# Optimization experiments

Measured on AMD Instinct MI355X. Metric: run time of the kernel, lower is better.

## Reference

```python
import jax, jax.numpy as jnp
import numpy as np

EPS = 1e-5  # torch LayerNorm default
NUM_HEADS = 8


def layernorm(x, g, b):
    m = jnp.mean(x, axis=-1, keepdims=True)
    v = jnp.var(x, axis=-1, keepdims=True)
    return (x - m) * jax.lax.rsqrt(v + EPS) * g + b


def dwconv(x_img, w, b):
    # x_img: [B,C,H,W]; w: [C,1,k,k] depthwise, 'same' padding
    C = x_img.shape[1]
    k = w.shape[-1]
    out = jax.lax.conv_general_dilated(
        x_img, w, (1, 1), [(k // 2, k // 2)] * 2,
        dimension_numbers=('NCHW', 'OIHW', 'NCHW'), feature_group_count=C)
    return out + b[None, :, None, None]


def _forward(x, domain_label, cpe_w, cpe_b, ln1_g, ln1_b, qkv_w, proj_w, proj_b,
             dl_w1, dl_b1, dl_w2, dl_b2, crpe_w3, crpe_b3, crpe_w5, crpe_b5,
             crpe_w7, crpe_b7, ln2_g, ln2_b, fc1_w, fc1_b, fc2_w, fc2_b, H, W, d):
    B, N, C = x.shape
    h = NUM_HEADS
    Ch = C // h
    scale = Ch ** (-0.5)

    # ---- CPE: depthwise 3x3 conv positional encoding with residual ----
    xi = x.transpose(0, 2, 1).reshape(B, C, H, W)
    xi = dwconv(xi, cpe_w, cpe_b) + xi
    x = xi.reshape(B, C, N).transpose(0, 2, 1)

    # ---- domain-indexed LayerNorm 1 (d is a static python int) ----
    cur = layernorm(x, ln1_g[d], ln1_b[d])

    # ---- factorized attention ----
    qkv = (cur @ qkv_w).reshape(B, N, 3, h, Ch).transpose(2, 0, 3, 1, 4)
    q, k, v = qkv[0], qkv[1], qkv[2]          # each [B,h,N,Ch]
    k_sm = jax.nn.softmax(k, axis=2)          # softmax over tokens
    kv = jnp.einsum('bhnk,bhnv->bhkv', k_sm, v)       # [B,h,Ch,Ch]
    factor_att = jnp.einsum('bhnk,bhkv->bhnv', q, kv)  # [B,h,N,Ch]

    # ---- conv relative position encoding (window splits {3:2,5:3,7:3}) ----
    v_img = v.transpose(0, 1, 3, 2).reshape(B, C, H, W)
    g1 = dwconv(v_img[:, :2 * Ch], crpe_w3, crpe_b3)
    g2 = dwconv(v_img[:, 2 * Ch:5 * Ch], crpe_w5, crpe_b5)
    g3 = dwconv(v_img[:, 5 * Ch:], crpe_w7, crpe_b7)
    conv_v = jnp.concatenate([g1, g2, g3], axis=1)        # [B,C,H,W]
    conv_v = conv_v.reshape(B, h, Ch, N).transpose(0, 1, 3, 2)
    crpe = q * conv_v                                      # [B,h,N,Ch]

    factor_att = scale * factor_att + crpe

    # ---- per-domain softmax gating over heads ----
    da = jax.nn.relu(domain_label @ dl_w1 + dl_b1) @ dl_w2 + dl_b2  # [B, h*Ch]
    da = da.reshape(B, h, Ch)[:, :, None, :]                        # [B,h,1,Ch]
    da = jax.nn.softmax(da, axis=1)                                  # over heads
    attn = (da * factor_att).transpose(0, 2, 1, 3).reshape(B, N, C)
    attn = attn @ proj_w + proj_b

    x = x + attn

    # ---- domain-indexed LayerNorm 2 + MLP ----
    cur = layernorm(x, ln2_g[d], ln2_b[d])
    cur = jax.nn.gelu(cur @ fc1_w + fc1_b, approximate=False) @ fc2_w + fc2_b
    return x + cur


def setup_inputs() -> dict:
    key = jax.random.key(0)
    ks = iter(jax.random.split(key, 32))
    B, H, W, C, h, nd = 8, 56, 56, 256, 8, 4
    N = H * W
    Ch = C // h
    hid = C // 2   # domain MLP hidden = max(dim//r,4), r=2
    mh = 4 * C     # mlp_ratio=4
    r = lambda shape, s=0.02: jax.random.normal(next(ks), shape, jnp.float32) * s
    return dict(
        x=jax.random.normal(next(ks), (B, N, C), jnp.float32),
        domain_label=jax.nn.one_hot(
            jax.random.randint(next(ks), (B,), 0, nd), nd, dtype=jnp.float32),
        cpe_w=r((C, 1, 3, 3)), cpe_b=jnp.zeros((C,), jnp.float32),
        ln1_g=jnp.ones((nd, C), jnp.float32), ln1_b=jnp.zeros((nd, C), jnp.float32),
        qkv_w=r((C, 3 * C)),
        proj_w=r((C, C)), proj_b=jnp.zeros((C,), jnp.float32),
        dl_w1=r((nd, hid)), dl_b1=jnp.zeros((hid,), jnp.float32),
        dl_w2=r((hid, C)), dl_b2=jnp.zeros((C,), jnp.float32),
        crpe_w3=r((2 * Ch, 1, 3, 3)), crpe_b3=jnp.zeros((2 * Ch,), jnp.float32),
        crpe_w5=r((3 * Ch, 1, 5, 5)), crpe_b5=jnp.zeros((3 * Ch,), jnp.float32),
        crpe_w7=r((3 * Ch, 1, 7, 7)), crpe_b7=jnp.zeros((3 * Ch,), jnp.float32),
        ln2_g=jnp.ones((nd, C), jnp.float32), ln2_b=jnp.zeros((nd, C), jnp.float32),
        fc1_w=r((C, mh)), fc1_b=jnp.zeros((mh,), jnp.float32),
        fc2_w=r((mh, C)), fc2_b=jnp.zeros((C,), jnp.float32),
        H=H, W=W, d=0,
    )


def reference(x, domain_label, cpe_w, cpe_b, ln1_g, ln1_b, qkv_w, proj_w, proj_b,
              dl_w1, dl_b1, dl_w2, dl_b2, crpe_w3, crpe_b3, crpe_w5, crpe_b5,
              crpe_w7, crpe_b7, ln2_g, ln2_b, fc1_w, fc1_b, fc2_w, fc2_b, H, W, d):
    return _forward(x, domain_label, cpe_w, cpe_b, ln1_g, ln1_b, qkv_w, proj_w,
                    proj_b, dl_w1, dl_b1, dl_w2, dl_b2, crpe_w3, crpe_b3, crpe_w5,
                    crpe_b5, crpe_w7, crpe_b7, ln2_g, ln2_b, fc1_w, fc1_b, fc2_w,
                    fc2_b, H, W, d)
```

## Files before the change

kernel.cpp:

```cpp
#include <hip/hip_runtime.h>
#include <hip/hip_bf16.h>
#include <math.h>

#define BB 8
#define HH 56
#define WW 56
#define NN (HH*WW)
#define CC 256
#define NH 8
#define NT (BB*NN)
#define HID 128
#define MH 1024
#define SCALE 0.17677669529663687f

typedef __attribute__((ext_vector_type(8))) short bf16x8;
typedef __attribute__((ext_vector_type(4))) float f32x4;

__device__ __forceinline__ ushort f2bf(float f) {
    __hip_bfloat16 h = __float2bfloat16(f);
    return *(ushort*)&h;
}
__device__ __forceinline__ uint pk2(float lo, float hi) {
    return ((uint)f2bf(hi) << 16) | (uint)f2bf(lo);
}
__device__ __forceinline__ float unlo(uint u) { return __uint_as_float(u << 16); }
__device__ __forceinline__ float unhi(uint u) { return __uint_as_float(u & 0xFFFF0000u); }

__device__ __forceinline__ void gload16(const void* g, void* s) {
    __builtin_amdgcn_global_load_lds(
        (const __attribute__((address_space(1))) void*)g,
        (__attribute__((address_space(3))) void*)s, 16, 0, 0);
}

__global__ __launch_bounds__(256) void wtrans_kernel(
    const float* __restrict__ w, ushort* __restrict__ wt, int K, int N)
{
    int idx = blockIdx.x * 256 + threadIdx.x;
    if (idx >= K * N) return;
    int n = idx / K, k = idx - n * K;
    wt[idx] = f2bf(w[(size_t)k * N + n]);
}

__global__ __launch_bounds__(256) void cpe_kernel(
    const float* __restrict__ x, const float* __restrict__ w,
    const float* __restrict__ bias, float* __restrict__ out)
{
    __shared__ uint vt[3 * 34 * 32];
    const int qq = blockIdx.x >> 1, hx = blockIdx.x & 1;
    const int y = blockIdx.y, b = blockIdx.z;
    const int c0 = qq * 64, x0 = hx * 28;
    const int t = threadIdx.x;
    const int p = t & 31;
    for (int rr = 0; rr < 3; ++rr) {
        int gy = y + rr - 1;
        const float* src = x + ((size_t)b * NN + gy * 56) * CC + c0;
        for (int lc = t >> 5; lc < 34; lc += 8) {
            int gx = x0 + lc - 3;
            float vlo = 0.f, vhi = 0.f;
            if ((unsigned)gy < 56u && (unsigned)gx < 56u) {
                vlo = src[(size_t)gx * CC + p];
                vhi = src[(size_t)gx * CC + p + 32];
            }
            vt[(rr * 34 + lc) * 32 + p] = pk2(vlo, vhi);
        }
    }
    uint wp[9];
    {
        const float* wl = w + (c0 + p) * 9;
        const float* wh = w + (c0 + 32 + p) * 9;
        #pragma unroll
        for (int i = 0; i < 9; ++i) wp[i] = pk2(wl[i], wh[i]);
    }
    const float blo = bias[c0 + p], bhi = bias[c0 + 32 + p];
    __syncthreads();

    const int wv = t >> 6, th = (t >> 5) & 1;
    int txl[4]; float clo[4], chi[4];
    #pragma unroll
    for (int jj = 0; jj < 4; ++jj) {
        int j = wv + jj * 4; if (j > 13) j = 13;
        txl[jj] = 2 * j + th;
        clo[jj] = blo; chi[jj] = bhi;
    }
    #pragma unroll
    for (int dy = 0; dy < 3; ++dy)
        #pragma unroll
        for (int dx = 0; dx < 3; ++dx) {
            const uint wpk = wp[dy * 3 + dx];
            const float wl = unlo(wpk), wh = unhi(wpk);
            #pragma unroll
            for (int jj = 0; jj < 4; ++jj) {
                uint vv = vt[(dy * 34 + txl[jj] + 2 + dx) * 32 + p];
                clo[jj] = fmaf(unlo(vv), wl, clo[jj]);
                chi[jj] = fmaf(unhi(vv), wh, chi[jj]);
            }
        }
    #pragma unroll
    for (int jj = 0; jj < 4; ++jj) {
        size_t tokg = (size_t)b * NN + y * 56 + x0 + txl[jj];
        const float* row = x + tokg * CC;
        out[tokg * CC + c0 + p]      = clo[jj] + row[c0 + p];
        out[tokg * CC + c0 + 32 + p] = chi[jj] + row[c0 + 32 + p];
    }
}

__global__ __launch_bounds__(256) void ln_kernel(
    const float* __restrict__ src, const float* __restrict__ g_all,
    const float* __restrict__ b_all, const int* __restrict__ dptr,
    ushort* __restrict__ dst)
{
    const int wid = threadIdx.x >> 6, lane = threadIdx.x & 63;
    const int row = blockIdx.x * 4 + wid;
    const int d = *dptr;
    const float* g = g_all + d * CC;
    const float* be = b_all + d * CC;
    const float* p = src + (size_t)row * CC;
    float4 v = *(const float4*)(p + lane * 4);
    float s = v.x + v.y + v.z + v.w;
    float sq = v.x*v.x + v.y*v.y + v.z*v.z + v.w*v.w;
    #pragma unroll
    for (int off = 1; off < 64; off <<= 1) {
        s  += __shfl_xor(s, off);
        sq += __shfl_xor(sq, off);
    }
    const float mean = s * (1.f / CC);
    const float var = sq * (1.f / CC) - mean * mean;
    const float rs = rsqrtf(var + 1e-5f);
    float4 g4 = *(const float4*)(g + lane * 4);
    float4 b4 = *(const float4*)(be + lane * 4);
    ushort4 o4;
    o4.x = f2bf((v.x - mean) * rs * g4.x + b4.x);
    o4.y = f2bf((v.y - mean) * rs * g4.y + b4.y);
    o4.z = f2bf((v.z - mean) * rs * g4.z + b4.z);
    o4.w = f2bf((v.w - mean) * rs * g4.w + b4.w);
    *(ushort4*)(dst + (size_t)row * CC + lane * 4) = o4;
}

template<int EPI>
__global__ __launch_bounds__(256) void gemm_mfma(
    const ushort* __restrict__ A, const ushort* __restrict__ Bt,
    const float* __restrict__ bias, const float* __restrict__ res,
    void* __restrict__ Cv, int M, int N, int K)
{
    __shared__ __align__(16) ushort Als[128 * 32];
    __shared__ __align__(16) ushort Bls[128 * 32];
    const int t = threadIdx.x;
    const int bm = blockIdx.y, bn = blockIdx.x;
    const int brow = bm * 128, bcol = bn * 128;
    const int lane = t & 63, w = t >> 6;
    const int wr = w >> 1, wc = w & 1;
    const int lrow = lane & 15, lko = (lane >> 4) * 8;

    const ushort* gA0 = A + (size_t)(brow + (t >> 2)) * K + (t & 3) * 8;
    const ushort* gA1 = gA0 + (size_t)64 * K;
    const ushort* gB0 = Bt + (size_t)(bcol + (t >> 2)) * K + (t & 3) * 8;
    const ushort* gB1 = gB0 + (size_t)64 * K;
    ushort* lA0 = &Als[t * 8];  ushort* lA1 = &Als[64 * 32 + t * 8];
    ushort* lB0 = &Bls[t * 8];  ushort* lB1 = &Bls[64 * 32 + t * 8];

    f32x4 acc[4][4] = {};

    for (int kt = 0; kt < K; kt += 32) {
        gload16(gA0 + kt, lA0);
        gload16(gA1 + kt, lA1);
        gload16(gB0 + kt, lB0);
        gload16(gB1 + kt, lB1);
        __syncthreads();
        bf16x8 af[4], bfr[4];
        #pragma unroll
        for (int i = 0; i < 4; ++i)
            af[i] = *(const bf16x8*)&Als[(wr * 64 + i * 16 + lrow) * 32 + lko];
        #pragma unroll
        for (int j = 0; j < 4; ++j)
            bfr[j] = *(const bf16x8*)&Bls[(wc * 64 + j * 16 + lrow) * 32 + lko];
        #pragma unroll
        for (int i = 0; i < 4; ++i)
            #pragma unroll
            for (int j = 0; j < 4; ++j)
                acc[i][j] = __builtin_amdgcn_mfma_f32_16x16x32_bf16(
                    af[i], bfr[j], acc[i][j], 0, 0, 0);
        __syncthreads();
    }

    float* Cf = (float*)Cv;
    ushort* Ch = (ushort*)Cv;
    #pragma unroll
    for (int j = 0; j < 4; ++j) {
        const int col = bcol + wc * 64 + j * 16 + lrow;
        const float bv = (EPI >= 2) ? bias[col] : 0.f;
        #pragma unroll
        for (int i = 0; i < 4; ++i) {
            const int row0 = brow + wr * 64 + i * 16 + (lane >> 4) * 4;
            #pragma unroll
            for (int r = 0; r < 4; ++r) {
                float v = acc[i][j][r] + bv;
                size_t off = (size_t)(row0 + r) * N + col;
                if (EPI == 2) {
                    v = 0.5f * v * (1.f + erff(v * 0.70710678118654752f));
                    Ch[off] = f2bf(v);
                } else if (EPI == 3) {
                    Cf[off] = v + res[off];
                } else {
                    Cf[off] = v;
                }
            }
        }
    }
}

__global__ __launch_bounds__(256) void kmax1_kernel(
    const float* __restrict__ qkv, float* __restrict__ pmax)
{
    const int chunk = blockIdx.x, b = blockIdx.y, c = threadIdx.x;
    const float* kb = qkv + (size_t)(b * NN + chunk * 98) * 768 + 256 + c;
    float m = -3.4e38f;
    for (int i = 0; i < 98; ++i) m = fmaxf(m, kb[(size_t)i * 768]);
    pmax[(b * 32 + chunk) * CC + c] = m;
}

__global__ __launch_bounds__(256) void kmax2_kernel(
    const float* __restrict__ pmax, float* __restrict__ cmax)
{
    const int b = blockIdx.x, c = threadIdx.x;
    float m = -3.4e38f;
    #pragma unroll
    for (int i = 0; i < 32; ++i) m = fmaxf(m, pmax[(b * 32 + i) * CC + c]);
    cmax[b * CC + c] = m;
}

__global__ __launch_bounds__(256) void kvacc_kernel(
    const float* __restrict__ qkv, const float* __restrict__ cmax,
    float* __restrict__ partial, float* __restrict__ psum)
{
    const int chunk = blockIdx.x, h = blockIdx.y, b = blockIdx.z;
    const int t = threadIdx.x;
    const int ck = t & 31, g = t >> 5;
    const int n0 = chunk * 196;
    const float* kb = qkv + (size_t)(b * NN + n0) * 768 + 256 + h * 32 + ck;
    const float* vb = qkv + (size_t)(b * NN + n0) * 768 + 512 + h * 32 + g * 4;
    const float cm = cmax[b * CC + h * 32 + ck];
    float a0 = 0.f, a1 = 0.f, a2 = 0.f, a3 = 0.f, s = 0.f;
    for (int i = 0; i < 196; ++i) {
        float e = __expf(kb[(size_t)i * 768] - cm);
        float4 v4 = *(const float4*)(vb + (size_t)i * 768);
        a0 += e * v4.x; a1 += e * v4.y; a2 += e * v4.z; a3 += e * v4.w;
        s += e;
    }
    float4 o = {a0, a1, a2, a3};
    *(float4*)(partial + ((((size_t)chunk * 8 + b) * 8 + h) * 32 + ck) * 32 + g * 4) = o;
    if (g == 0) psum[((chunk * 8 + b) * 8 + h) * 32 + ck] = s;
}

__global__ __launch_bounds__(256) void kvnorm_kernel(
    const float* __restrict__ partial, const float* __restrict__ psum,
    float* __restrict__ kv)
{
    const int idx = blockIdx.x * 256 + threadIdx.x;
    const int ckidx = idx >> 5;
    float sum = 0.f, cs = 0.f;
    #pragma unroll
    for (int ch = 0; ch < 16; ++ch) {
        sum += partial[(size_t)ch * 65536 + idx];
        cs  += psum[ch * 2048 + ckidx];
    }
    kv[idx] = sum / cs;
}

__global__ __launch_bounds__(256) void fa_kernel(
    float* __restrict__ qkv, const float* __restrict__ kvb)
{
    const int mt = blockIdx.x, h = blockIdx.y, b = blockIdx.z;
    const int t = threadIdx.x;
    const int lane = t & 63, wv = t >> 6;
    const int row0 = mt * 448 + wv * 112;
    const int lr = lane & 15, lk = (lane >> 4) * 8;

    bf16x8 bfr[2];
    #pragma unroll
    for (int jj = 0; jj < 2; ++jj)
        #pragma unroll
        for (int e = 0; e < 8; ++e)
            bfr[jj][e] = (short)f2bf(kvb[((size_t)(b * 8 + h) * 32 + lk + e) * 32 + jj * 16 + lr]);

    #pragma unroll
    for (int i = 0; i < 7; ++i) {
        size_t tok = (size_t)b * NN + row0 + i * 16 + lr;
        const float* qp = qkv + tok * 768 + h * 32 + lk;
        float4 qa = *(const float4*)qp;
        float4 qb2 = *(const float4*)(qp + 4);
        bf16x8 af;
        af[0] = (short)f2bf(qa.x);  af[1] = (short)f2bf(qa.y);
        af[2] = (short)f2bf(qa.z);  af[3] = (short)f2bf(qa.w);
        af[4] = (short)f2bf(qb2.x); af[5] = (short)f2bf(qb2.y);
        af[6] = (short)f2bf(qb2.z); af[7] = (short)f2bf(qb2.w);
        f32x4 a0 = {0.f, 0.f, 0.f, 0.f}, a1 = {0.f, 0.f, 0.f, 0.f};
        a0 = __builtin_amdgcn_mfma_f32_16x16x32_bf16(af, bfr[0], a0, 0, 0, 0);
        a1 = __builtin_amdgcn_mfma_f32_16x16x32_bf16(af, bfr[1], a1, 0, 0, 0);
        #pragma unroll
        for (int r = 0; r < 4; ++r) {
            size_t trow = (size_t)b * NN + row0 + i * 16 + (lane >> 4) * 4 + r;
            qkv[trow * 768 + 256 + h * 32 + lr]      = a0[r];
            qkv[trow * 768 + 256 + h * 32 + 16 + lr] = a1[r];
        }
    }
}

__global__ __launch_bounds__(256) void da_kernel(
    const float* __restrict__ dl, const float* __restrict__ w1,
    const float* __restrict__ b1, const float* __restrict__ w2,
    const float* __restrict__ b2, float* __restrict__ da)
{
    const int b = blockIdx.x, t = threadIdx.x;
    __shared__ float r[HID];
    __shared__ float raw[CC];
    if (t < HID) {
        float s = b1[t];
        #pragma unroll
        for (int k = 0; k < 4; ++k) s += dl[b * 4 + k] * w1[k * HID + t];
        r[t] = fmaxf(s, 0.f);
    }
    __syncthreads();
    float s = b2[t];
    for (int j = 0; j < HID; ++j) s += r[j] * w2[j * CC + t];
    raw[t] = s;
    __syncthreads();
    const int ch = t & 31;
    float m = -3.4e38f;
    #pragma unroll
    for (int hh = 0; hh < NH; ++hh) m = fmaxf(m, raw[hh * 32 + ch]);
    float ssum = 0.f;
    #pragma unroll
    for (int hh = 0; hh < NH; ++hh) ssum += __expf(raw[hh * 32 + ch] - m);
    da[b * CC + t] = __expf(raw[t] - m) / ssum;
}

template<int KS, int KSLO>
__device__ __forceinline__ void comb_body(
    uint* vt, int c0,
    const float* __restrict__ wlo_base, const float* __restrict__ whi_base,
    const float* __restrict__ blo_base, const float* __restrict__ bhi_base,
    const float* __restrict__ qkv, const float* __restrict__ da,
    ushort* __restrict__ out)
{
    constexpr int R = KS / 2, OFF = R - KSLO / 2;
    const int hx = blockIdx.x & 1, y = blockIdx.y, b = blockIdx.z;
    const int x0 = hx * 28;
    const int t = threadIdx.x;
    const int p = t & 31;
    for (int rr = 0; rr < KS; ++rr) {
        int gy = y + rr - R;
        const float* src = qkv + ((size_t)b * NN + gy * 56) * 768 + 512 + c0;
        for (int lc = t >> 5; lc < 34; lc += 8) {
            int gx = x0 + lc - 3;
            float vlo = 0.f, vhi = 0.f;
            if ((unsigned)gy < 56u && (unsigned)gx < 56u) {
                vlo = src[(size_t)gx * 768 + p];
                vhi = src[(size_t)gx * 768 + p + 32];
            }
            vt[(rr * 34 + lc) * 32 + p] = pk2(vlo, vhi);
        }
    }
    uint wp[KS * KS];
    {
        const float* wl = wlo_base + p * (KSLO * KSLO);
        const float* wh = whi_base + p * (KS * KS);
        #pragma unroll
        for (int dy = 0; dy < KS; ++dy)
            #pragma unroll
            for (int dx = 0; dx < KS; ++dx) {
                float lo = 0.f;
                if (dy >= OFF && dy < OFF + KSLO && dx >= OFF && dx < OFF + KSLO)
                    lo = wl[(dy - OFF) * KSLO + (dx - OFF)];
                wp[dy * KS + dx] = pk2(lo, wh[dy * KS + dx]);
            }
    }
    const float blo = blo_base[p], bhi = bhi_base[p];
    const float dalo = da[b * CC + c0 + p], dahi = da[b * CC + c0 + 32 + p];
    __syncthreads();

    const int wv = t >> 6, th = (t >> 5) & 1;
    int txl[4]; float clo[4], chi[4];
    #pragma unroll
    for (int jj = 0; jj < 4; ++jj) {
        int j = wv + jj * 4; if (j > 13) j = 13;
        txl[jj] = 2 * j + th;
        clo[jj] = blo; chi[jj] = bhi;
    }
    #pragma unroll
    for (int dy = 0; dy < KS; ++dy)
        #pragma unroll
        for (int dx = 0; dx < KS; ++dx) {
            const uint wpk = wp[dy * KS + dx];
            const float wl = unlo(wpk), wh = unhi(wpk);
            #pragma unroll
            for (int jj = 0; jj < 4; ++jj) {
                uint vv = vt[(dy * 34 + txl[jj] + 3 - R + dx) * 32 + p];
                clo[jj] = fmaf(unlo(vv), wl, clo[jj]);
                chi[jj] = fmaf(unhi(vv), wh, chi[jj]);
            }
        }
    #pragma unroll
    for (int jj = 0; jj < 4; ++jj) {
        size_t tokg = (size_t)b * NN + y * 56 + x0 + txl[jj];
        const float* row = qkv + tokg * 768;
        float fal = row[256 + c0 + p], fah = row[256 + c0 + 32 + p];
        float ql = row[c0 + p], qh = row[c0 + 32 + p];
        out[tokg * CC + c0 + p]      = f2bf(dalo * (SCALE * fal + ql * clo[jj]));
        out[tokg * CC + c0 + 32 + p] = f2bf(dahi * (SCALE * fah + qh * chi[jj]));
    }
}

__global__ __launch_bounds__(256) void combine_kernel(
    const float* __restrict__ qkv, const float* __restrict__ da,
    const float* __restrict__ w3, const float* __restrict__ b3,
    const float* __restrict__ w5, const float* __restrict__ b5,
    const float* __restrict__ w7, const float* __restrict__ b7,
    ushort* __restrict__ out)
{
    __shared__ uint vt[7 * 34 * 32];
    switch (blockIdx.x >> 1) {
    case 0: comb_body<3,3>(vt, 0,   w3,           w3 + 32*9,  b3,      b3 + 32, qkv, da, out); break;
    case 1: comb_body<5,5>(vt, 64,  w5,           w5 + 32*25, b5,      b5 + 32, qkv, da, out); break;
    case 2: comb_body<7,5>(vt, 128, w5 + 64*25,   w7,         b5 + 64, b7,      qkv, da, out); break;
    default: comb_body<7,7>(vt, 192, w7 + 32*49,  w7 + 64*49, b7 + 32, b7 + 64, qkv, da, out); break;
    }
}

extern "C" void kernel_launch(void* const* d_in, const int* in_sizes, int n_in,
                              void* d_out, int out_size, void* d_ws, size_t ws_size,
                              hipStream_t stream)
{
    const float* x       = (const float*)d_in[0];
    const float* dlab    = (const float*)d_in[1];
    const float* cpe_w   = (const float*)d_in[2];
    const float* cpe_b   = (const float*)d_in[3];
    const float* ln1_g   = (const float*)d_in[4];
    const float* ln1_b   = (const float*)d_in[5];
    const float* qkv_w   = (const float*)d_in[6];
    const float* proj_w  = (const float*)d_in[7];
    const float* proj_b  = (const float*)d_in[8];
    const float* dl_w1   = (const float*)d_in[9];
    const float* dl_b1   = (const float*)d_in[10];
    const float* dl_w2   = (const float*)d_in[11];
    const float* dl_b2   = (const float*)d_in[12];
    const float* crpe_w3 = (const float*)d_in[13];
    const float* crpe_b3 = (const float*)d_in[14];
    const float* crpe_w5 = (const float*)d_in[15];
    const float* crpe_b5 = (const float*)d_in[16];
    const float* crpe_w7 = (const float*)d_in[17];
    const float* crpe_b7 = (const float*)d_in[18];
    const float* ln2_g   = (const float*)d_in[19];
    const float* ln2_b   = (const float*)d_in[20];
    const float* fc1_w   = (const float*)d_in[21];
    const float* fc1_b   = (const float*)d_in[22];
    const float* fc2_w   = (const float*)d_in[23];
    const float* fc2_b   = (const float*)d_in[24];
    const int*   dptr    = (const int*)d_in[27];

    float* out = (float*)d_out;
    char* W = (char*)d_ws;
    size_t off = 0;
    float* x1 = (float*)(W + off);          off += (size_t)NT * CC * 4;
    float* qkv = (float*)(W + off);
    ushort* hidden = (ushort*)qkv;
    off += (size_t)NT * 768 * 4;
    ushort* actbf = (ushort*)(W + off);     off += (size_t)NT * CC * 2;
    float* partial = (float*)actbf;
    float* psum = partial + (size_t)16 * 65536;
    float* kvb = (float*)(W + off);         off += (size_t)65536 * 4;
    float* dab = (float*)(W + off);         off += (size_t)BB * CC * 4;
    float* pmax = (float*)(W + off);        off += (size_t)BB * 32 * CC * 4;
    float* cmax = (float*)(W + off);        off += (size_t)BB * CC * 4;
    ushort* wq  = (ushort*)(W + off);       off += (size_t)768 * 256 * 2;
    ushort* wp  = (ushort*)(W + off);       off += (size_t)256 * 256 * 2;
    ushort* w1t = (ushort*)(W + off);       off += (size_t)1024 * 256 * 2;
    ushort* w2t = (ushort*)(W + off);       off += (size_t)256 * 1024 * 2;

    hipLaunchKernelGGL(wtrans_kernel, dim3(768), dim3(256), 0, stream, qkv_w, wq, 256, 768);
    hipLaunchKernelGGL(wtrans_kernel, dim3(256), dim3(256), 0, stream, proj_w, wp, 256, 256);
    hipLaunchKernelGGL(wtrans_kernel, dim3(1024), dim3(256), 0, stream, fc1_w, w1t, 256, 1024);
    hipLaunchKernelGGL(wtrans_kernel, dim3(1024), dim3(256), 0, stream, fc2_w, w2t, 1024, 256);
    hipLaunchKernelGGL(cpe_kernel, dim3(8, 56, 8), dim3(256), 0, stream, x, cpe_w, cpe_b, x1);
    hipLaunchKernelGGL(da_kernel, dim3(BB), dim3(256), 0, stream,
                       dlab, dl_w1, dl_b1, dl_w2, dl_b2, dab);
    hipLaunchKernelGGL(ln_kernel, dim3(NT / 4), dim3(256), 0, stream,
                       x1, ln1_g, ln1_b, dptr, actbf);
    hipLaunchKernelGGL(gemm_mfma<0>, dim3(768 / 128, NT / 128), dim3(256), 0, stream,
                       actbf, wq, nullptr, nullptr, (void*)qkv, NT, 768, 256);
    hipLaunchKernelGGL(kmax1_kernel, dim3(32, 8), dim3(256), 0, stream, qkv, pmax);
    hipLaunchKernelGGL(kmax2_kernel, dim3(8), dim3(256), 0, stream, pmax, cmax);
    hipLaunchKernelGGL(kvacc_kernel, dim3(16, 8, 8), dim3(256), 0, stream,
                       qkv, cmax, partial, psum);
    hipLaunchKernelGGL(kvnorm_kernel, dim3(256), dim3(256), 0, stream,
                       partial, psum, kvb);
    hipLaunchKernelGGL(fa_kernel, dim3(7, 8, 8), dim3(256), 0, stream, qkv, kvb);
    hipLaunchKernelGGL(combine_kernel, dim3(8, 56, 8), dim3(256), 0, stream,
                       qkv, dab, crpe_w3, crpe_b3, crpe_w5, crpe_b5,
                       crpe_w7, crpe_b7, actbf);
    hipLaunchKernelGGL(gemm_mfma<3>, dim3(256 / 128, NT / 128), dim3(256), 0, stream,
                       actbf, wp, proj_b, x1, (void*)out, NT, 256, 256);
    hipLaunchKernelGGL(ln_kernel, dim3(NT / 4), dim3(256), 0, stream,
                       out, ln2_g, ln2_b, dptr, actbf);
    hipLaunchKernelGGL(gemm_mfma<2>, dim3(1024 / 128, NT / 128), dim3(256), 0, stream,
                       actbf, w1t, fc1_b, nullptr, (void*)hidden, NT, 1024, 256);
    hipLaunchKernelGGL(gemm_mfma<3>, dim3(256 / 128, NT / 128), dim3(256), 0, stream,
                       hidden, w2t, fc2_b, out, (void*)out, NT, 256, 1024);
}
```

Before: 437.4 us.

## Register-tile depthwise convs over two rows and seven columns, vectorize loads, tile weight transpose

The CPE and CRPE depthwise conv kernels now handle two output rows per block. Each thread computes seven adjacent columns for a pair of interleaved channels, reusing a sliding register window of LDS values rather than reloading them per tap. Halo loads become float4 and stores float2, which cuts redundant LDS and global traffic. The weight transpose now uses a shared-memory 32x32 tile so global reads and writes are coalesced. In exchange, register pressure rises and channel-to-kernel-size selection moves to per-thread runtime branches.

Measured after the change: 439.0 us. No clear change (+0.4%).

```diff
diff --git a/kernel.cpp b/kernel.cpp
--- a/kernel.cpp
+++ b/kernel.cpp
@@ -35,72 +35,87 @@
 __global__ __launch_bounds__(256) void wtrans_kernel(
     const float* __restrict__ w, ushort* __restrict__ wt, int K, int N)
 {
-    int idx = blockIdx.x * 256 + threadIdx.x;
-    if (idx >= K * N) return;
-    int n = idx / K, k = idx - n * K;
-    wt[idx] = f2bf(w[(size_t)k * N + n]);
+    __shared__ float tile[32][33];
+    const int t = threadIdx.x;
+    const int col = t & 31, rw = t >> 5;
+    const int k0 = blockIdx.y * 32, n0 = blockIdx.x * 32;
+    #pragma unroll
+    for (int i = rw; i < 32; i += 8)
+        tile[i][col] = w[(size_t)(k0 + i) * N + n0 + col];
+    __syncthreads();
+    #pragma unroll
+    for (int i = rw; i < 32; i += 8)
+        wt[(size_t)(n0 + i) * K + k0 + col] = f2bf(tile[col][i]);
 }
 
 __global__ __launch_bounds__(256) void cpe_kernel(
     const float* __restrict__ x, const float* __restrict__ w,
     const float* __restrict__ bias, float* __restrict__ out)
 {
-    __shared__ uint vt[3 * 34 * 32];
+    __shared__ uint vt[4 * 34 * 32];
     const int qq = blockIdx.x >> 1, hx = blockIdx.x & 1;
-    const int y = blockIdx.y, b = blockIdx.z;
-    const int c0 = qq * 64, x0 = hx * 28;
+    const int y0 = blockIdx.y * 2, b = blockIdx.z;
+    const int x0 = hx * 28;
     const int t = threadIdx.x;
-    const int p = t & 31;
-    for (int rr = 0; rr < 3; ++rr) {
-        int gy = y + rr - 1;
-        const float* src = x + ((size_t)b * NN + gy * 56) * CC + c0;
-        for (int lc = t >> 5; lc < 34; lc += 8) {
-            int gx = x0 + lc - 3;
-            float vlo = 0.f, vhi = 0.f;
-            if ((unsigned)gy < 56u && (unsigned)gx < 56u) {
-                vlo = src[(size_t)gx * CC + p];
-                vhi = src[(size_t)gx * CC + p + 32];
+    const int c0 = qq * 64;
+
+    {
+        const int cw = t & 15, cg = t >> 4;
+        for (int pos = cw; pos < 4 * 34; pos += 16) {
+            int row = pos / 34, col = pos - row * 34;
+            int gy = y0 + row - 1, gx = x0 + col - 3;
+            float4 v = {0.f, 0.f, 0.f, 0.f};
+            if ((unsigned)gy < 56u && (unsigned)gx < 56u)
+                v = *(const float4*)(x + ((size_t)b * NN + gy * 56 + gx) * CC + c0 + cg * 4);
+            uint2 pk = { pk2(v.x, v.y), pk2(v.z, v.w) };
+            *(uint2*)&vt[pos * 32 + cg * 2] = pk;
+        }
+    }
+    const int p = t & 31, rseg = t >> 5;
+    const int r = rseg >> 2, sg = rseg & 3;
+    const int cA = c0 + 2 * p;
+    uint wpk[9];
+    {
+        const float* wA = w + cA * 9;
+        const float* wB = wA + 9;
+        #pragma unroll
+        for (int i = 0; i < 9; ++i) wpk[i] = pk2(wA[i], wB[i]);
+    }
+    const float cbA = bias[cA], cbB = bias[cA + 1];
+    __syncthreads();
+
+    float accA[7], accB[7];
+    #pragma unroll
+    for (int k = 0; k < 7; ++k) { accA[k] = cbA; accB[k] = cbB; }
+
+    #pragma unroll
+    for (int dy = 0; dy < 3; ++dy) {
+        const int rowbase = (r + dy) * 34 * 32;
+        float fA[9], fB[9];
+        #pragma unroll
+        for (int u = 0; u < 9; ++u) {
+            uint vv = vt[rowbase + (sg * 7 + 2 + u) * 32 + p];
+            fA[u] = unlo(vv); fB[u] = unhi(vv);
+        }
+        #pragma unroll
+        for (int dx = 0; dx < 3; ++dx) {
+            uint wv = wpk[dy * 3 + dx];
+            float wl = unlo(wv), wh = unhi(wv);
+            #pragma unroll
+            for (int k = 0; k < 7; ++k) {
+                accA[k] = fmaf(fA[dx + k], wl, accA[k]);
+                accB[k] = fmaf(fB[dx + k], wh, accB[k]);
             }
-            vt[(rr * 34 + lc) * 32 + p] = pk2(vlo, vhi);
-        }
-    }
-    uint wp[9];
-    {
-        const float* wl = w + (c0 + p) * 9;
-        const float* wh = w + (c0 + 32 + p) * 9;
-        #pragma unroll
-        for (int i = 0; i < 9; ++i) wp[i] = pk2(wl[i], wh[i]);
-    }
-    const float blo = bias[c0 + p], bhi = bias[c0 + 32 + p];
-    __syncthreads();
-
-    const int wv = t >> 6, th = (t >> 5) & 1;
-    int txl[4]; float clo[4], chi[4];
-    #pragma unroll
-    for (int jj = 0; jj < 4; ++jj) {
-        int j = wv + jj * 4; if (j > 13) j = 13;
-        txl[jj] = 2 * j + th;
-        clo[jj] = blo; chi[jj] = bhi;
-    }
-    #pragma unroll
-    for (int dy = 0; dy < 3; ++dy)
-        #pragma unroll
-        for (int dx = 0; dx < 3; ++dx) {
-            const uint wpk = wp[dy * 3 + dx];
-            const float wl = unlo(wpk), wh = unhi(wpk);
-            #pragma unroll
-            for (int jj = 0; jj < 4; ++jj) {
-                uint vv = vt[(dy * 34 + txl[jj] + 2 + dx) * 32 + p];
-                clo[jj] = fmaf(unlo(vv), wl, clo[jj]);
-                chi[jj] = fmaf(unhi(vv), wh, chi[jj]);
-            }
-        }
-    #pragma unroll
-    for (int jj = 0; jj < 4; ++jj) {
-        size_t tokg = (size_t)b * NN + y * 56 + x0 + txl[jj];
-        const float* row = x + tokg * CC;
-        out[tokg * CC + c0 + p]      = clo[jj] + row[c0 + p];
-        out[tokg * CC + c0 + 32 + p] = chi[jj] + row[c0 + 32 + p];
+        }
+    }
+
+    const int ytok = y0 + r;
+    #pragma unroll
+    for (int k = 0; k < 7; ++k) {
+        size_t tok = (size_t)b * NN + ytok * 56 + x0 + sg * 7 + k;
+        float2 res = *(const float2*)(x + tok * CC + cA);
+        float2 o = { accA[k] + res.x, accB[k] + res.y };
+        *(float2*)(out + tok * CC + cA) = o;
     }
 }
 
@@ -334,79 +349,94 @@
     da[b * CC + t] = __expf(raw[t] - m) / ssum;
 }
 
-template<int KS, int KSLO>
+template<int KS>
 __device__ __forceinline__ void comb_body(
-    uint* vt, int c0,
-    const float* __restrict__ wlo_base, const float* __restrict__ whi_base,
-    const float* __restrict__ blo_base, const float* __restrict__ bhi_base,
+    uint* vt, int qq,
     const float* __restrict__ qkv, const float* __restrict__ da,
+    const float* __restrict__ w3, const float* __restrict__ b3,
+    const float* __restrict__ w5, const float* __restrict__ b5,
+    const float* __restrict__ w7, const float* __restrict__ b7,
     ushort* __restrict__ out)
 {
-    constexpr int R = KS / 2, OFF = R - KSLO / 2;
-    const int hx = blockIdx.x & 1, y = blockIdx.y, b = blockIdx.z;
+    constexpr int R = KS / 2;
+    constexpr int TR = KS + 1;
+    constexpr int WCOLS = 7 + 2 * R;
+    const int hx = blockIdx.x & 1;
+    const int y0 = blockIdx.y * 2, b = blockIdx.z;
     const int x0 = hx * 28;
     const int t = threadIdx.x;
-    const int p = t & 31;
-    for (int rr = 0; rr < KS; ++rr) {
-        int gy = y + rr - R;
-        const float* src = qkv + ((size_t)b * NN + gy * 56) * 768 + 512 + c0;
-        for (int lc = t >> 5; lc < 34; lc += 8) {
-            int gx = x0 + lc - 3;
-            float vlo = 0.f, vhi = 0.f;
-            if ((unsigned)gy < 56u && (unsigned)gx < 56u) {
-                vlo = src[(size_t)gx * 768 + p];
-                vhi = src[(size_t)gx * 768 + p + 32];
+    const int c0 = qq * 64;
+
+    {
+        const int cw = t & 15, cg = t >> 4;
+        for (int pos = cw; pos < TR * 34; pos += 16) {
+            int row = pos / 34, col = pos - row * 34;
+            int gy = y0 + row - R, gx = x0 + col - 3;
+            float4 v = {0.f, 0.f, 0.f, 0.f};
+            if ((unsigned)gy < 56u && (unsigned)gx < 56u)
+                v = *(const float4*)(qkv + ((size_t)b * NN + gy * 56 + gx) * 768 + 512 + c0 + cg * 4);
+            uint2 pk = { pk2(v.x, v.y), pk2(v.z, v.w) };
+            *(uint2*)&vt[pos * 32 + cg * 2] = pk;
+        }
+    }
+    const int p = t & 31, rseg = t >> 5;
+    const int r = rseg >> 2, sg = rseg & 3;
+    const int cA = c0 + 2 * p;
+    int rK; const float* wbA; const float* wbB; float cbA, cbB;
+    if (cA < 64)       { rK = 1; wbA = w3 + cA * 9;          wbB = wbA + 9;  cbA = b3[cA];       cbB = b3[cA + 1]; }
+    else if (cA < 160) { rK = 2; wbA = w5 + (cA - 64) * 25;  wbB = wbA + 25; cbA = b5[cA - 64];  cbB = b5[cA - 63]; }
+    else               { rK = 3; wbA = w7 + (cA - 160) * 49; wbB = wbA + 49; cbA = b7[cA - 160]; cbB = b7[cA - 159]; }
+    const int kslo = 2 * rK + 1, offp = R - rK;
+    uint wpk[KS * KS];
+    #pragma unroll
+    for (int dy = 0; dy < KS; ++dy)
+        #pragma unroll
+        for (int dx = 0; dx < KS; ++dx) {
+            float lo = 0.f, hi = 0.f;
+            int sy = dy - offp, sx = dx - offp;
+            if (sy >= 0 && sy < kslo && sx >= 0 && sx < kslo) {
+                lo = wbA[sy * kslo + sx];
+                hi = wbB[sy * kslo + sx];
             }
-            vt[(rr * 34 + lc) * 32 + p] = pk2(vlo, vhi);
-        }
-    }
-    uint wp[KS * KS];
-    {
-        const float* wl = wlo_base + p * (KSLO * KSLO);
-        const float* wh = whi_base + p * (KS * KS);
-        #pragma unroll
-        for (int dy = 0; dy < KS; ++dy)
+            wpk[dy * KS + dx] = pk2(lo, hi);
+        }
+    __syncthreads();
+
+    float accA[7], accB[7];
+    #pragma unroll
+    for (int k = 0; k < 7; ++k) { accA[k] = cbA; accB[k] = cbB; }
+
+    #pragma unroll
+    for (int dy = 0; dy < KS; ++dy) {
+        const int rowbase = (r + dy) * 34 * 32;
+        float fA[WCOLS], fB[WCOLS];
+        #pragma unroll
+        for (int u = 0; u < WCOLS; ++u) {
+            uint vv = vt[rowbase + (sg * 7 + 3 - R + u) * 32 + p];
+            fA[u] = unlo(vv); fB[u] = unhi(vv);
+        }
+        #pragma unroll
+        for (int dx = 0; dx < KS; ++dx) {
+            uint wv = wpk[dy * KS + dx];
+            float wl = unlo(wv), wh = unhi(wv);
             #pragma unroll
-            for (int dx = 0; dx < KS; ++dx) {
-                float lo = 0.f;
-                if (dy >= OFF && dy < OFF + KSLO && dx >= OFF && dx < OFF + KSLO)
-                    lo = wl[(dy - OFF) * KSLO + (dx - OFF)];
-                wp[dy * KS + dx] = pk2(lo, wh[dy * KS + dx]);
+            for (int k = 0; k < 7; ++k) {
+                accA[k] = fmaf(fA[dx + k], wl, accA[k]);
+                accB[k] = fmaf(fB[dx + k], wh, accB[k]);
             }
-    }
-    const float blo = blo_base[p], bhi = bhi_base[p];
-    const float dalo = da[b * CC + c0 + p], dahi = da[b * CC + c0 + 32 + p];
-    __syncthreads();
-
-    const int wv = t >> 6, th = (t >> 5) & 1;
-    int txl[4]; float clo[4], chi[4];
-    #pragma unroll
-    for (int jj = 0; jj < 4; ++jj) {
-        int j = wv + jj * 4; if (j > 13) j = 13;
-        txl[jj] = 2 * j + th;
-        clo[jj] = blo; chi[jj] = bhi;
-    }
-    #pragma unroll
-    for (int dy = 0; dy < KS; ++dy)
-        #pragma unroll
-        for (int dx = 0; dx < KS; ++dx) {
-            const uint wpk = wp[dy * KS + dx];
-            const float wl = unlo(wpk), wh = unhi(wpk);
-            #pragma unroll
-            for (int jj = 0; jj < 4; ++jj) {
-                uint vv = vt[(dy * 34 + txl[jj] + 3 - R + dx) * 32 + p];
-                clo[jj] = fmaf(unlo(vv), wl, clo[jj]);
-                chi[jj] = fmaf(unhi(vv), wh, chi[jj]);
-            }
-        }
-    #pragma unroll
-    for (int jj = 0; jj < 4; ++jj) {
-        size_t tokg = (size_t)b * NN + y * 56 + x0 + txl[jj];
-        const float* row = qkv + tokg * 768;
-        float fal = row[256 + c0 + p], fah = row[256 + c0 + 32 + p];
-        float ql = row[c0 + p], qh = row[c0 + 32 + p];
-        out[tokg * CC + c0 + p]      = f2bf(dalo * (SCALE * fal + ql * clo[jj]));
-        out[tokg * CC + c0 + 32 + p] = f2bf(dahi * (SCALE * fah + qh * chi[jj]));
+        }
+    }
+
+    const float daA = da[b * CC + cA], daB = da[b * CC + cA + 1];
+    const int ytok = y0 + r;
+    #pragma unroll
+    for (int k = 0; k < 7; ++k) {
+        size_t tok = (size_t)b * NN + ytok * 56 + x0 + sg * 7 + k;
+        float2 q2 = *(const float2*)(qkv + tok * 768 + cA);
+        float2 fa2 = *(const float2*)(qkv + tok * 768 + 256 + cA);
+        ushort2 o = { f2bf(daA * (SCALE * fa2.x + q2.x * accA[k])),
+                      f2bf(daB * (SCALE * fa2.y + q2.y * accB[k])) };
+        *(ushort2*)(out + tok * CC + cA) = o;
     }
 }
 
@@ -417,12 +447,12 @@
     const float* __restrict__ w7, const float* __restrict__ b7,
     ushort* __restrict__ out)
 {
-    __shared__ uint vt[7 * 34 * 32];
+    __shared__ uint vt[8 * 34 * 32];
     switch (blockIdx.x >> 1) {
-    case 0: comb_body<3,3>(vt, 0,   w3,           w3 + 32*9,  b3,      b3 + 32, qkv, da, out); break;
-    case 1: comb_body<5,5>(vt, 64,  w5,           w5 + 32*25, b5,      b5 + 32, qkv, da, out); break;
-    case 2: comb_body<7,5>(vt, 128, w5 + 64*25,   w7,         b5 + 64, b7,      qkv, da, out); break;
-    default: comb_body<7,7>(vt, 192, w7 + 32*49,  w7 + 64*49, b7 + 32, b7 + 64, qkv, da, out); break;
+    case 0:  comb_body<3>(vt, 0, qkv, da, w3, b3, w5, b5, w7, b7, out); break;
+    case 1:  comb_body<5>(vt, 1, qkv, da, w3, b3, w5, b5, w7, b7, out); break;
+    case 2:  comb_body<7>(vt, 2, qkv, da, w3, b3, w5, b5, w7, b7, out); break;
+    default: comb_body<7>(vt, 3, qkv, da, w3, b3, w5, b5, w7, b7, out); break;
     }
 }
 
@@ -476,11 +506,11 @@
     ushort* w1t = (ushort*)(W + off);       off += (size_t)1024 * 256 * 2;
     ushort* w2t = (ushort*)(W + off);       off += (size_t)256 * 1024 * 2;
 
-    hipLaunchKernelGGL(wtrans_kernel, dim3(768), dim3(256), 0, stream, qkv_w, wq, 256, 768);
-    hipLaunchKernelGGL(wtrans_kernel, dim3(256), dim3(256), 0, stream, proj_w, wp, 256, 256);
-    hipLaunchKernelGGL(wtrans_kernel, dim3(1024), dim3(256), 0, stream, fc1_w, w1t, 256, 1024);
-    hipLaunchKernelGGL(wtrans_kernel, dim3(1024), dim3(256), 0, stream, fc2_w, w2t, 1024, 256);
-    hipLaunchKernelGGL(cpe_kernel, dim3(8, 56, 8), dim3(256), 0, stream, x, cpe_w, cpe_b, x1);
+    hipLaunchKernelGGL(wtrans_kernel, dim3(768 / 32, 256 / 32), dim3(256), 0, stream, qkv_w, wq, 256, 768);
+    hipLaunchKernelGGL(wtrans_kernel, dim3(256 / 32, 256 / 32), dim3(256), 0, stream, proj_w, wp, 256, 256);
+    hipLaunchKernelGGL(wtrans_kernel, dim3(1024 / 32, 256 / 32), dim3(256), 0, stream, fc1_w, w1t, 256, 1024);
+    hipLaunchKernelGGL(wtrans_kernel, dim3(256 / 32, 1024 / 32), dim3(256), 0, stream, fc2_w, w2t, 1024, 256);
+    hipLaunchKernelGGL(cpe_kernel, dim3(8, 28, 8), dim3(256), 0, stream, x, cpe_w, cpe_b, x1);
     hipLaunchKernelGGL(da_kernel, dim3(BB), dim3(256), 0, stream,
                        dlab, dl_w1, dl_b1, dl_w2, dl_b2, dab);
     hipLaunchKernelGGL(ln_kernel, dim3(NT / 4), dim3(256), 0, stream,
@@ -494,7 +524,7 @@
     hipLaunchKernelGGL(kvnorm_kernel, dim3(256), dim3(256), 0, stream,
                        partial, psum, kvb);
     hipLaunchKernelGGL(fa_kernel, dim3(7, 8, 8), dim3(256), 0, stream, qkv, kvb);
-    hipLaunchKernelGGL(combine_kernel, dim3(8, 56, 8), dim3(256), 0, stream,
+    hipLaunchKernelGGL(combine_kernel, dim3(8, 28, 8), dim3(256), 0, stream,
                        qkv, dab, crpe_w3, crpe_b3, crpe_w5, crpe_b5,
                        crpe_w7, crpe_b7, actbf);
     hipLaunchKernelGGL(gemm_mfma<3>, dim3(256 / 128, NT / 128), dim3(256), 0, stream,
```
